# Kernel optimization log

Hardware: AMD Instinct MI355X
Metric: run time of the kernel (lower is better)

The kernel has to match this reference:

```python
import jax, jax.numpy as jnp
import numpy as np

N = 6144      # total residues (12 complexes x 512)
SEG = 512
NC = 14       # atom channels per residue
E = 64        # embed_size
HD = 128      # hidden_size
C = 25        # num_classes
K = 9         # k_neighbors
L = 3         # n_layers
ROUNDS = 3    # iter_round


def _forward(X, S, batch_id, embed, W_in, b_in, channel_w, eW1, eb1, eW2, eb2, cW1, cb1, cW2, cb2, nW1, nb1, nW2, nb2, mW1, mb1, mW2, mb2, oW1, ob1, oW2, ob2):
    n = X.shape[0]
    silu = jax.nn.silu
    # pairs in different complexes (or self) are never neighbors
    cross = (batch_id[:, None] != batch_id[None, :]) | jnp.eye(n, dtype=bool)
    Hmem = None
    H = None
    for t in range(ROUNDS):
        H0 = embed[S]                                    # residue embedding [N,E]
        if Hmem is not None:                             # keep_memory: memory_ffn(H_prev)
            m = silu(Hmem) @ mW1 + mb1
            H0 = H0 + (silu(m) @ mW2 + mb2)
        H = H0 @ W_in + b_in                             # [N,HD]
        # dynamic KNN edge construction on current CA coordinates (_knn_edges)
        ca = X[:, 1]                                     # [N,3]
        d2 = jnp.sum((ca[:, None, :] - ca[None, :, :]) ** 2, -1)
        d2 = jnp.where(cross, 1e9, d2)
        _, nbr = jax.lax.top_k(-d2, K)                   # [N,K] neighbor indices
        for l in range(L):                               # AMEGNN / AMEncoder layers
            Hj = H[nbr]                                  # gather [N,K,HD]
            Xj = X[nbr]                                  # gather [N,K,NC,3]
            diff = X[:, None] - Xj                       # [N,K,NC,3]
            # channel-weighted radial feature
            radial = jnp.einsum('nkcd,nkcd,c->nk', diff, diff, channel_w)[..., None]
            Hi = jnp.broadcast_to(H[:, None], Hj.shape)
            ein = jnp.concatenate([Hi, Hj, radial], -1)  # [N,K,2HD+1]
            msg = silu(silu(ein @ eW1[l] + eb1[l]) @ eW2[l] + eb2[l])
            scale = silu(msg @ cW1[l] + cb1[l]) @ cW2[l] + cb2[l]     # [N,K,1]
            X = X + jnp.mean(diff * scale[..., None], axis=1)        # equivariant coord update
            agg = jnp.sum(msg, axis=1)                   # scatter-sum over neighbors [N,HD]
            H = H + silu(jnp.concatenate([H, agg], -1) @ nW1[l] + nb1[l]) @ nW2[l] + nb2[l]
        Hmem = H
    logits = silu(silu(H) @ oW1 + ob1) @ oW2 + ob2       # ffn_residue
    return logits, X


def setup_inputs() -> dict:
    key = jax.random.key(0)
    ks = jax.random.split(key, 16)
    r = lambda i, shape, s=0.05: jax.random.normal(ks[i], shape, dtype=jnp.float32) * s
    return {
        'X': jax.random.normal(ks[0], (N, NC, 3), dtype=jnp.float32) * 3.0,
        'S': jax.random.randint(ks[1], (N,), 0, C),
        'batch_id': jnp.arange(N, dtype=jnp.int32) // SEG,
        'embed': r(2, (C, E), 1.0),
        'W_in': r(3, (E, HD)), 'b_in': jnp.zeros((HD,), jnp.float32),
        'channel_w': jax.random.uniform(ks[4], (NC,), dtype=jnp.float32),
        'eW1': r(5, (L, 2 * HD + 1, HD)), 'eb1': jnp.zeros((L, HD), jnp.float32),
        'eW2': r(6, (L, HD, HD)), 'eb2': jnp.zeros((L, HD), jnp.float32),
        'cW1': r(7, (L, HD, HD)), 'cb1': jnp.zeros((L, HD), jnp.float32),
        'cW2': r(8, (L, HD, 1)), 'cb2': jnp.zeros((L, 1), jnp.float32),
        'nW1': r(9, (L, 2 * HD, HD)), 'nb1': jnp.zeros((L, HD), jnp.float32),
        'nW2': r(10, (L, HD, HD)), 'nb2': jnp.zeros((L, HD), jnp.float32),
        'mW1': r(11, (HD, HD)), 'mb1': jnp.zeros((HD,), jnp.float32),
        'mW2': r(12, (HD, E)), 'mb2': jnp.zeros((E,), jnp.float32),
        'oW1': r(13, (HD, HD)), 'ob1': jnp.zeros((HD,), jnp.float32),
        'oW2': r(14, (HD, C)), 'ob2': jnp.zeros((C,), jnp.float32),
    }


def reference(X, S, batch_id, embed, W_in, b_in, channel_w, eW1, eb1, eW2, eb2, cW1, cb1, cW2, cb2, nW1, nb1, nW2, nb2, mW1, mb1, mW2, mb2, oW1, ob1, oW2, ob2):
    return _forward(X, S, batch_id, embed, W_in, b_in, channel_w, eW1, eb1, eW2, eb2, cW1, cb1, cW2, cb2, nW1, nb1, nW2, nb2, mW1, mb1, mW2, mb2, oW1, ob1, oW2, ob2)
```

## Files before the change

kernel.cpp:

```cpp
#include <hip/hip_runtime.h>
#include <hip/hip_bf16.h>
#include <math.h>

#define NNODE 6144
#define SEG   512
#define NCH   14
#define XD    42
#define ED    64
#define HD    128
#define NCLS  25
#define KN    9
#define NPB   7
#define ROWS  64
#define EDGE_BLOCKS ((NNODE + NPB - 1) / NPB)

typedef __attribute__((ext_vector_type(8))) short short8;
typedef __attribute__((ext_vector_type(4))) short short4v;
typedef __attribute__((ext_vector_type(4))) float f32x4;

__device__ __forceinline__ float silu_f(float x) {
  return x / (1.0f + __expf(-x));
}
__device__ __forceinline__ short f2bf(float x) {
  __hip_bfloat16 h = __float2bfloat16(x);
  return __builtin_bit_cast(short, h);
}
__device__ __forceinline__ unsigned pkbf(float lo, float hi) {
  return (unsigned)(unsigned short)f2bf(lo)
       | ((unsigned)(unsigned short)f2bf(hi) << 16);
}
__device__ __forceinline__ float bf2f(short s) {
  unsigned u = ((unsigned)(unsigned short)s) << 16;
  return __builtin_bit_cast(float, u);
}
__device__ __forceinline__ f32x4 mfma16(short8 a, short8 b, f32x4 c) {
  return __builtin_amdgcn_mfma_f32_16x16x32_bf16(a, b, c, 0, 0, 0);
}
__device__ __forceinline__ int swz128(int row, int col) {
  return row * 128 + (col ^ ((row & 7) << 3));
}
__device__ __forceinline__ int swz256(int row, int col) {
  return row * 256 + (col ^ ((row & 7) << 3));
}
__device__ __forceinline__ int swz64(int row, int col) {
  return row * 64 + (col ^ ((row & 7) << 3));
}

#define EXOFF 344064
#define WBF_SHORTS (EXOFF + 32768)

__global__ __launch_bounds__(256) void prep_weights(
    const float* __restrict__ eW1, const float* __restrict__ eW2,
    const float* __restrict__ cW1, const float* __restrict__ nW1,
    const float* __restrict__ nW2, const float* __restrict__ mW1,
    const float* __restrict__ mW2, const float* __restrict__ W_in,
    short* __restrict__ out)
{
  const int idx = blockIdx.x * 256 + threadIdx.x;
  if (blockIdx.y == 15) {
    if (idx < 16384) {
      const int n = idx >> 7, k = idx & 127;
      out[EXOFF + idx] = f2bf(mW1[k * HD + n]);
    } else if (idx < 24576) {
      const int local = idx - 16384;
      const int n = local >> 7, k = local & 127;
      out[EXOFF + 16384 + local] = f2bf(mW2[k * ED + n]);
    } else if (idx < 32768) {
      const int local = idx - 24576;
      const int n = local >> 6, k = local & 63;
      out[EXOFF + 24576 + local] = f2bf(W_in[k * HD + n]);
    }
    return;
  }
  const int mat = blockIdx.y % 5, l = blockIdx.y / 5;
  const int K = (mat == 0 || mat == 3) ? 256 : 128;
  if (idx >= K * 128) return;
  const int n = idx / K, k = idx - n * K;
  const float* src;
  switch (mat) {
    case 0: src = eW1 + (size_t)l * 257 * 128; break;
    case 1: src = eW2 + (size_t)l * 128 * 128; break;
    case 2: src = cW1 + (size_t)l * 128 * 128; break;
    case 3: src = nW1 + (size_t)l * 256 * 128; break;
    default: src = nW2 + (size_t)l * 128 * 128; break;
  }
  const int dofs[5] = {0, 32768, 49152, 65536, 98304};
  out[(size_t)l * 114688 + dofs[mat] + idx] = f2bf(src[k * 128 + n]);
}

__global__ void copy_kernel(const float* __restrict__ src, float* __restrict__ dst, int n) {
  int i = blockIdx.x * blockDim.x + threadIdx.x;
  if (i < n) dst[i] = src[i];
}

__global__ __launch_bounds__(512) void h_init_mfma(
    const float* __restrict__ embed, const int* __restrict__ S,
    const short* __restrict__ W_inT, const float* __restrict__ b_in,
    const float* __restrict__ Hmem,
    const short* __restrict__ mW1T, const float* __restrict__ mb1,
    const short* __restrict__ mW2T, const float* __restrict__ mb2,
    const short* __restrict__ W1T0,
    float* __restrict__ Hout, short* __restrict__ PQ0)
{
  __shared__ __align__(16) short A[16 * HD];
  __shared__ __align__(16) short Bu[16 * HD];
  __shared__ __align__(16) short h0B[16 * ED];
  __shared__ __align__(16) short HB[16 * HD];
  const int t = threadIdx.x;
  const int m0 = blockIdx.x * 16;
  const int wid = t >> 6, lane = t & 63, lr = lane & 15, lk = lane >> 4;

  if (Hmem) {
    {
      const int r = t >> 5, c4 = t & 31;
      const float4 v = ((const float4*)Hmem)[(size_t)(m0 + r) * 32 + c4];
      uint2 u;
      u.x = pkbf(silu_f(v.x), silu_f(v.y));
      u.y = pkbf(silu_f(v.z), silu_f(v.w));
      *(uint2*)&A[swz128(r, c4 * 4)] = u;
    }
    __syncthreads();
    {
      f32x4 acc[2] = {};
#pragma unroll
      for (int ks = 0; ks < 4; ++ks) {
        const int k0 = ks * 32 + lk * 8;
        const short8 a = *(const short8*)&A[swz128(lr, k0)];
#pragma unroll
        for (int ni = 0; ni < 2; ++ni) {
          const int c = (wid * 2 + ni) * 16 + lr;
          acc[ni] = mfma16(a, *(const short8*)(mW1T + c * 128 + k0), acc[ni]);
        }
      }
#pragma unroll
      for (int ni = 0; ni < 2; ++ni) {
        const int col = (wid * 2 + ni) * 16 + lr;
        const float bias = mb1[col];
#pragma unroll
        for (int g = 0; g < 4; ++g)
          Bu[swz128(lk * 4 + g, col)] = f2bf(silu_f(acc[ni][g] + bias));
      }
    }
    __syncthreads();
    if (wid < 4) {
      f32x4 acc = {};
#pragma unroll
      for (int ks = 0; ks < 4; ++ks) {
        const int k0 = ks * 32 + lk * 8;
        const short8 a = *(const short8*)&Bu[swz128(lr, k0)];
        const int c = wid * 16 + lr;
        acc = mfma16(a, *(const short8*)(mW2T + c * 128 + k0), acc);
      }
      const int col = wid * 16 + lr;
      const float bias = mb2[col];
#pragma unroll
      for (int g = 0; g < 4; ++g) {
        const int row = lk * 4 + g;
        h0B[swz64(row, col)] = f2bf(embed[S[m0 + row] * ED + col] + acc[g] + bias);
      }
    }
  } else {
    for (int idx = t; idx < 16 * ED; idx += 512) {
      const int row = idx >> 6, col = idx & 63;
      h0B[swz64(row, col)] = f2bf(embed[S[m0 + row] * ED + col]);
    }
  }
  __syncthreads();
  {
    f32x4 acc = {};
#pragma unroll
    for (int ks = 0; ks < 2; ++ks) {
      const int k0 = ks * 32 + lk * 8;
      const short8 a = *(const short8*)&h0B[swz64(lr, k0)];
      const int c = wid * 16 + lr;
      acc = mfma16(a, *(const short8*)(W_inT + c * 64 + k0), acc);
    }
    const int col = wid * 16 + lr;
    const float bias = b_in[col];
#pragma unroll
    for (int g = 0; g < 4; ++g) {
      const int row = lk * 4 + g;
      const float hv = acc[g] + bias;
      Hout[(size_t)(m0 + row) * HD + col] = hv;
      HB[swz128(row, col)] = f2bf(hv);
    }
  }
  __syncthreads();
  {
    f32x4 acc[2] = {};
#pragma unroll
    for (int ks = 0; ks < 4; ++ks) {
      const int k0 = ks * 32 + lk * 8;
      const short8 a = *(const short8*)&HB[swz128(lr, k0)];
#pragma unroll
      for (int ni = 0; ni < 2; ++ni) {
        const int c = (wid * 2 + ni) * 16 + lr;
        const short* bp = (c < HD) ? (W1T0 + c * 256 + k0)
                                   : (W1T0 + (c - HD) * 256 + HD + k0);
        acc[ni] = mfma16(a, *(const short8*)bp, acc[ni]);
      }
    }
#pragma unroll
    for (int ni = 0; ni < 2; ++ni) {
      const int c = (wid * 2 + ni) * 16 + lr;
#pragma unroll
      for (int g = 0; g < 4; ++g)
        PQ0[(size_t)(m0 + lk * 4 + g) * 256 + c] = f2bf(acc[ni][g]);
    }
  }
}

__global__ __launch_bounds__(512) void knn_kernel(const float* __restrict__ X,
                                                  int* __restrict__ nbr)
{
  const int w = threadIdx.x >> 6, lane = threadIdx.x & 63;
  const int i = blockIdx.x * 8 + w;
  const int base = (i / SEG) * SEG;

  const float cx = X[i * XD + 3], cy = X[i * XD + 4], cz = X[i * XD + 5];
  float dv[8];
  int   di[8];
#pragma unroll
  for (int q = 0; q < 8; ++q) {
    const int j = base + lane + q * 64;
    float dx = __fsub_rn(cx, X[j * XD + 3]);
    float dy = __fsub_rn(cy, X[j * XD + 4]);
    float dz = __fsub_rn(cz, X[j * XD + 5]);
    float d2 = __fadd_rn(__fadd_rn(__fmul_rn(dx, dx), __fmul_rn(dy, dy)), __fmul_rn(dz, dz));
    if (j == i) d2 = 1e9f;
    dv[q] = d2; di[q] = j;
  }
  for (int it = 0; it < KN; ++it) {
    float bv = dv[0]; int bi = di[0];
#pragma unroll
    for (int q = 1; q < 8; ++q)
      if (dv[q] < bv || (dv[q] == bv && di[q] < bi)) { bv = dv[q]; bi = di[q]; }
#pragma unroll
    for (int m = 1; m < 64; m <<= 1) {
      float ov = __shfl_xor(bv, m, 64);
      int   oi = __shfl_xor(bi, m, 64);
      if (ov < bv || (ov == bv && oi < bi)) { bv = ov; bi = oi; }
    }
    if (lane == 0) nbr[i * KN + it] = bi;
    const int rel = bi - base;
    const int oq = rel >> 6;
#pragma unroll
    for (int q = 0; q < 8; ++q)
      if (q == oq && (rel & 63) == lane) dv[q] = 3e38f;
  }
}

__global__ __launch_bounds__(512) void edge_layer_kernel(
    const float* __restrict__ Hin,  float* __restrict__ Hout,
    const float* __restrict__ Xin,  float* __restrict__ Xout,
    const int*   __restrict__ nbr,  const float* __restrict__ channel_w,
    const short* __restrict__ PQ,
    const float* __restrict__ eW1,  const float* __restrict__ eb1,
    const float* __restrict__ eb2,  const float* __restrict__ cb1,
    const float* __restrict__ cW2,  const float* __restrict__ cb2,
    const float* __restrict__ nb1,  const float* __restrict__ nb2,
    const short* __restrict__ W2T,  const short* __restrict__ C1T,
    const short* __restrict__ N1T,  const short* __restrict__ N2T,
    const short* __restrict__ W1Tn, short* __restrict__ PQn)
{
  __shared__ __align__(16) short bufA[ROWS * HD];
  __shared__ __align__(16) short bufB[ROWS * HD];
  __shared__ __align__(16) short nodeA[NPB * 256];
  __shared__ __align__(16) short uT[NPB * HD];
  __shared__ float scalePart[ROWS][4];
  __shared__ int   nbrS[ROWS];
  short* houtB = bufA;

  const int t  = threadIdx.x;
  const int n0 = blockIdx.x * NPB;
  const int nvalid = (NNODE - n0 < NPB) ? (NNODE - n0) : NPB;
  const int evalid = nvalid * KN;

  {
    const int row  = t >> 3;
    const int part = t & 7;
    const bool rvalid = row < evalid;
    const int nd = row / KN;
    const int jn = rvalid ? nbr[n0 * KN + row] : n0;
    if (part == 0) nbrS[row] = jn;

    float r = 0.f;
    {
      const float* xi = Xin + (size_t)(n0 + ((nd < nvalid) ? nd : 0)) * XD;
      const float* xj = Xin + (size_t)jn * XD;
#pragma unroll
      for (int ii = 0; ii < 6; ++ii) {
        const int e = part + ii * 8;
        if (e < XD) {
          float d = 0.f;
          if (rvalid) d = xi[e] - xj[e];
          r = fmaf(channel_w[e / 3] * d, d, r);
        }
      }
    }
    r += __shfl_xor(r, 1, 64);
    r += __shfl_xor(r, 2, 64);
    r += __shfl_xor(r, 4, 64);

    if (t < NPB * (HD / 4)) {
      const int r2 = t >> 5, c4 = t & 31;
      float4 v = make_float4(0.f, 0.f, 0.f, 0.f);
      if (r2 < nvalid) v = ((const float4*)Hin)[(size_t)(n0 + r2) * 32 + c4];
      uint2 u;
      u.x = pkbf(v.x, v.y);
      u.y = pkbf(v.z, v.w);
      *(uint2*)&nodeA[swz256(r2, c4 * 4)] = u;
    }

    const int inode = n0 + ((nd < nvalid) ? nd : 0);
    const short4v* PQv = (const short4v*)PQ;
    const float4* w2564 = (const float4*)(eW1 + 256 * HD);
    const float4* eb14 = (const float4*)eb1;
#pragma unroll
    for (int ii = 0; ii < 4; ++ii) {
      const int c4 = part + ii * 8;
      const short4v ps = PQv[(size_t)inode * 64 + c4];
      const short4v qs = PQv[(size_t)jn * 64 + 32 + c4];
      const float4 w = w2564[c4];
      const float4 bb = eb14[c4];
      uint2 u;
      u.x = pkbf(silu_f(bf2f(ps.x) + bf2f(qs.x) + r * w.x + bb.x),
                 silu_f(bf2f(ps.y) + bf2f(qs.y) + r * w.y + bb.y));
      u.y = pkbf(silu_f(bf2f(ps.z) + bf2f(qs.z) + r * w.z + bb.z),
                 silu_f(bf2f(ps.w) + bf2f(qs.w) + r * w.w + bb.w));
      *(uint2*)&bufA[swz128(row, c4 * 4)] = u;
    }
  }
  __syncthreads();

  const int wid  = t >> 6;
  const int lane = t & 63;
  const int m2 = wid >> 2;
  const int n2 = wid & 3;
  const int lr = lane & 15;
  const int lk = lane >> 4;
  const int rA0 = (m2 * 2) * 16 + lr;
  const int rA1 = rA0 + 16;

  {
    f32x4 acc[2][2] = {};
    const short* b0p = W2T + ((n2 * 2) * 16 + lr) * 128;
    const short* b1p = b0p + 16 * 128;
#pragma unroll
    for (int ks = 0; ks < 4; ++ks) {
      const int k0 = ks * 32 + lk * 8;
      const short8 a0 = *(const short8*)&bufA[swz128(rA0, k0)];
      const short8 a1 = *(const short8*)&bufA[swz128(rA1, k0)];
      const short8 b0 = *(const short8*)(b0p + k0);
      const short8 b1 = *(const short8*)(b1p + k0);
      acc[0][0] = mfma16(a0, b0, acc[0][0]);
      acc[0][1] = mfma16(a0, b1, acc[0][1]);
      acc[1][0] = mfma16(a1, b0, acc[1][0]);
      acc[1][1] = mfma16(a1, b1, acc[1][1]);
    }
#pragma unroll
    for (int ni = 0; ni < 2; ++ni) {
      const int col = (n2 * 2 + ni) * 16 + lr;
      const float bias = eb2[col];
#pragma unroll
      for (int mi = 0; mi < 2; ++mi) {
        const int rb = (m2 * 2 + mi) * 16 + lk * 4;
#pragma unroll
        for (int g = 0; g < 4; ++g)
          bufB[swz128(rb + g, col)] = f2bf(silu_f(acc[mi][ni][g] + bias));
      }
    }
  }
  __syncthreads();

  {
    f32x4 acc[2][2] = {};
    const short* b0p = C1T + ((n2 * 2) * 16 + lr) * 128;
    const short* b1p = b0p + 16 * 128;
#pragma unroll
    for (int ks = 0; ks < 4; ++ks) {
      const int k0 = ks * 32 + lk * 8;
      const short8 a0 = *(const short8*)&bufB[swz128(rA0, k0)];
      const short8 a1 = *(const short8*)&bufB[swz128(rA1, k0)];
      const short8 b0 = *(const short8*)(b0p + k0);
      const short8 b1 = *(const short8*)(b1p + k0);
      acc[0][0] = mfma16(a0, b0, acc[0][0]);
      acc[0][1] = mfma16(a0, b1, acc[0][1]);
      acc[1][0] = mfma16(a1, b0, acc[1][0]);
      acc[1][1] = mfma16(a1, b1, acc[1][1]);
    }
    float p[2][4];
#pragma unroll
    for (int mi = 0; mi < 2; ++mi)
#pragma unroll
      for (int g = 0; g < 4; ++g) p[mi][g] = 0.f;
#pragma unroll
    for (int ni = 0; ni < 2; ++ni) {
      const int col = (n2 * 2 + ni) * 16 + lr;
      const float bias = cb1[col];
      const float wv = cW2[col];
#pragma unroll
      for (int mi = 0; mi < 2; ++mi)
#pragma unroll
        for (int g = 0; g < 4; ++g)
          p[mi][g] = fmaf(silu_f(acc[mi][ni][g] + bias), wv, p[mi][g]);
    }
#pragma unroll
    for (int m = 1; m < 16; m <<= 1) {
#pragma unroll
      for (int mi = 0; mi < 2; ++mi)
#pragma unroll
        for (int g = 0; g < 4; ++g)
          p[mi][g] += __shfl_xor(p[mi][g], m, 64);
    }
    if (lr == 0) {
#pragma unroll
      for (int mi = 0; mi < 2; ++mi)
#pragma unroll
        for (int g = 0; g < 4; ++g)
          scalePart[(m2 * 2 + mi) * 16 + lk * 4 + g][n2] = p[mi][g];
    }
  }
  if (t < NPB * (HD / 2)) {
    const int r2 = t >> 6, cp = (t & 63) * 2;
    float v0 = 0.f, v1 = 0.f;
#pragma unroll
    for (int k = 0; k < KN; ++k) {
      const unsigned w = *(const unsigned*)&bufB[swz128(r2 * KN + k, cp)];
      v0 += bf2f((short)(w & 0xffffu));
      v1 += bf2f((short)(w >> 16));
    }
    if (r2 >= nvalid) { v0 = 0.f; v1 = 0.f; }
    *(unsigned*)&nodeA[swz256(r2, cp + HD)] = pkbf(v0, v1);
  }
  __syncthreads();

  {
    f32x4 acc = {};
    const short* bp = N1T + (wid * 16 + lr) * 256;
#pragma unroll
    for (int ks = 0; ks < 8; ++ks) {
      const int k0 = ks * 32 + lk * 8;
      short8 a = {0, 0, 0, 0, 0, 0, 0, 0};
      if (lr < NPB) a = *(const short8*)&nodeA[swz256(lr, k0)];
      const short8 b = *(const short8*)(bp + k0);
      acc = mfma16(a, b, acc);
    }
    const int col = wid * 16 + lr;
    const float bias = nb1[col];
#pragma unroll
    for (int g = 0; g < 4; ++g) {
      const int orow = lk * 4 + g;
      if (orow < NPB) uT[swz128(orow, col)] = f2bf(silu_f(acc[g] + bias));
    }
  }
  if (t < NPB * XD) {
    const int nd = t / XD, e = t - nd * XD;
    if (nd < nvalid) {
      const float c2 = cb2[0];
      const float xi = Xin[(size_t)n0 * XD + t];
      float a = 0.f;
#pragma unroll
      for (int k = 0; k < KN; ++k) {
        const int r = nd * KN + k;
        const float sc = ((scalePart[r][0] + scalePart[r][1])
                        + (scalePart[r][2] + scalePart[r][3])) + c2;
        a = fmaf(xi - Xin[(size_t)nbrS[r] * XD + e], sc, a);
      }
      Xout[(size_t)n0 * XD + t] = xi + a / 9.0f;
    }
  }
  __syncthreads();

  {
    f32x4 acc = {};
    const short* bp = N2T + (wid * 16 + lr) * 128;
#pragma unroll
    for (int ks = 0; ks < 4; ++ks) {
      const int k0 = ks * 32 + lk * 8;
      short8 a = {0, 0, 0, 0, 0, 0, 0, 0};
      if (lr < NPB) a = *(const short8*)&uT[swz128(lr, k0)];
      const short8 b = *(const short8*)(bp + k0);
      acc = mfma16(a, b, acc);
    }
    const int col = wid * 16 + lr;
    const float bias = nb2[col];
#pragma unroll
    for (int g = 0; g < 4; ++g) {
      const int row = lk * 4 + g;
      if (row < nvalid) {
        const float hv = Hin[(size_t)(n0 + row) * HD + col] + acc[g] + bias;
        Hout[(size_t)(n0 + row) * HD + col] = hv;
        if (W1Tn) houtB[swz128(row, col)] = f2bf(hv);
      }
    }
  }

  if (W1Tn) {
    __syncthreads();
    f32x4 acc[2] = {};
#pragma unroll
    for (int ks = 0; ks < 4; ++ks) {
      const int k0 = ks * 32 + lk * 8;
      short8 a = {0, 0, 0, 0, 0, 0, 0, 0};
      if (lr < NPB) a = *(const short8*)&houtB[swz128(lr, k0)];
#pragma unroll
      for (int ni = 0; ni < 2; ++ni) {
        const int c = (wid * 2 + ni) * 16 + lr;
        const short* bp = (c < HD) ? (W1Tn + c * 256 + k0)
                                   : (W1Tn + (c - HD) * 256 + HD + k0);
        acc[ni] = mfma16(a, *(const short8*)bp, acc[ni]);
      }
    }
#pragma unroll
    for (int ni = 0; ni < 2; ++ni) {
      const int c = (wid * 2 + ni) * 16 + lr;
#pragma unroll
      for (int g = 0; g < 4; ++g) {
        const int row = lk * 4 + g;
        if (row < nvalid) PQn[(size_t)(n0 + row) * 256 + c] = f2bf(acc[ni][g]);
      }
    }
  }
}

__global__ __launch_bounds__(128) void out_kernel(
    const float* __restrict__ H, const float* __restrict__ X,
    const float* __restrict__ oW1, const float* __restrict__ ob1,
    const float* __restrict__ oW2, const float* __restrict__ ob2,
    float* __restrict__ out)
{
  __shared__ float hs[HD];
  __shared__ float u[HD];
  const int i = blockIdx.x, j = threadIdx.x;

  hs[j] = silu_f(H[i * HD + j]);
  __syncthreads();
  float a0 = 0.f, a1 = 0.f, a2 = 0.f, a3 = 0.f;
  for (int k = 0; k < HD; k += 4) {
    a0 = fmaf(hs[k + 0], oW1[(k + 0) * HD + j], a0);
    a1 = fmaf(hs[k + 1], oW1[(k + 1) * HD + j], a1);
    a2 = fmaf(hs[k + 2], oW1[(k + 2) * HD + j], a2);
    a3 = fmaf(hs[k + 3], oW1[(k + 3) * HD + j], a3);
  }
  u[j] = silu_f(ob1[j] + ((a0 + a1) + (a2 + a3)));
  __syncthreads();
  if (j < NCLS) {
    float o0 = 0.f, o1 = 0.f, o2 = 0.f, o3 = 0.f;
    for (int k = 0; k < HD; k += 4) {
      o0 = fmaf(u[k + 0], oW2[(k + 0) * NCLS + j], o0);
      o1 = fmaf(u[k + 1], oW2[(k + 1) * NCLS + j], o1);
      o2 = fmaf(u[k + 2], oW2[(k + 2) * NCLS + j], o2);
      o3 = fmaf(u[k + 3], oW2[(k + 3) * NCLS + j], o3);
    }
    out[i * NCLS + j] = ob2[j] + ((o0 + o1) + (o2 + o3));
  }
  if (j < XD) out[NNODE * NCLS + i * XD + j] = X[i * XD + j];
}

extern "C" void kernel_launch(void* const* d_in, const int* in_sizes, int n_in,
                              void* d_out, int out_size, void* d_ws, size_t ws_size,
                              hipStream_t stream)
{
  const float* X0       = (const float*)d_in[0];
  const int*   S        = (const int*)  d_in[1];
  const float* embed    = (const float*)d_in[3];
  const float* W_in     = (const float*)d_in[4];
  const float* b_in     = (const float*)d_in[5];
  const float* channelw = (const float*)d_in[6];
  const float* eW1      = (const float*)d_in[7];
  const float* eb1      = (const float*)d_in[8];
  const float* eW2      = (const float*)d_in[9];
  const float* eb2      = (const float*)d_in[10];
  const float* cW1      = (const float*)d_in[11];
  const float* cb1      = (const float*)d_in[12];
  const float* cW2      = (const float*)d_in[13];
  const float* cb2      = (const float*)d_in[14];
  const float* nW1      = (const float*)d_in[15];
  const float* nb1      = (const float*)d_in[16];
  const float* nW2      = (const float*)d_in[17];
  const float* nb2      = (const float*)d_in[18];
  const float* mW1      = (const float*)d_in[19];
  const float* mb1      = (const float*)d_in[20];
  const float* mW2      = (const float*)d_in[21];
  const float* mb2      = (const float*)d_in[22];
  const float* oW1      = (const float*)d_in[23];
  const float* ob1      = (const float*)d_in[24];
  const float* oW2      = (const float*)d_in[25];
  const float* ob2      = (const float*)d_in[26];

  char* ws = (char*)d_ws;
  const size_t HBYTES = (size_t)NNODE * HD * sizeof(float);
  const size_t XBYTES = (size_t)NNODE * XD * sizeof(float);
  const size_t NBRB   = (size_t)NNODE * KN * sizeof(int);
  const size_t WBFB   = (size_t)WBF_SHORTS * sizeof(short);
  const size_t PQB    = (size_t)NNODE * 256 * sizeof(short);
  float* Hb[2] = { (float*)(ws), (float*)(ws + HBYTES) };
  float* Xb[2] = { (float*)(ws + 2 * HBYTES), (float*)(ws + 2 * HBYTES + XBYTES) };
  int*   nbr   = (int*)(ws + 2 * HBYTES + 2 * XBYTES);
  short* Wbf   = (short*)(ws + 2 * HBYTES + 2 * XBYTES + NBRB);
  short* PQb[2] = { (short*)(ws + 2 * HBYTES + 2 * XBYTES + NBRB + WBFB),
                    (short*)(ws + 2 * HBYTES + 2 * XBYTES + NBRB + WBFB + PQB) };

  prep_weights<<<dim3(128, 16), 256, 0, stream>>>(eW1, eW2, cW1, nW1, nW2,
                                                  mW1, mW2, W_in, Wbf);
  copy_kernel<<<(NNODE * XD + 255) / 256, 256, 0, stream>>>(X0, Xb[0], NNODE * XD);

  int hc = 0, xc = 0;
  for (int t = 0; t < 3; ++t) {
    const float* Hmem = (t == 0) ? nullptr : Hb[hc];
    h_init_mfma<<<NNODE / 16, 512, 0, stream>>>(
        embed, S, Wbf + EXOFF + 24576, b_in, Hmem,
        Wbf + EXOFF, mb1, Wbf + EXOFF + 16384, mb2,
        Wbf , Hb[hc ^ 1], PQb[0]);
    hc ^= 1;
    knn_kernel<<<NNODE / 8, 512, 0, stream>>>(Xb[xc], nbr);
    for (int l = 0; l < 3; ++l) {
      const short* Wl = Wbf + (size_t)l * 114688;
      const short* Wn = (l < 2) ? (Wbf + (size_t)(l + 1) * 114688) : nullptr;
      const short* pqr = (l == 1) ? PQb[1] : PQb[0];
      short* pqw = (l == 0) ? PQb[1] : ((l == 1) ? PQb[0] : nullptr);
      edge_layer_kernel<<<EDGE_BLOCKS, 512, 0, stream>>>(
          Hb[hc], Hb[hc ^ 1], Xb[xc], Xb[xc ^ 1], nbr, channelw, pqr,
          eW1 + (size_t)l * 257 * HD, eb1 + (size_t)l * HD,
          eb2 + (size_t)l * HD,  cb1 + (size_t)l * HD,
          cW2 + (size_t)l * HD,  cb2 + (size_t)l,
          nb1 + (size_t)l * HD,  nb2 + (size_t)l * HD,
          Wl + 32768, Wl + 49152, Wl + 65536, Wl + 98304,
          Wn, pqw);
      hc ^= 1; xc ^= 1;
    }
  }
  out_kernel<<<NNODE, HD, 0, stream>>>(Hb[hc], Xb[xc], oW1, ob1, oW2, ob2, (float*)d_out);
}
```

Measured before the change: 535.5 us.

## Shrink edge-layer blocks to 3 nodes, 256 threads, and rebalance MFMA tiling

Edge-layer blocks now handle 3 nodes (27 edge rows padded to 32) with 4 waves instead of 7 nodes (63 rows padded to 64) with 8 waves. The MFMA work split is remapped so each wave owns wider column strips, and the boundary checks go away because 6144 divides by 3 evenly. This cuts padding waste, raises block count and occupancy, and lowers LDS use per block. In exchange the per-block weight loads are amortised over fewer nodes, and the node-level MFMAs, which use only 3 of 16 A rows, waste more tensor work. SiLU also now uses a reciprocal multiply in place of a divide.

Result: slower. 702.6 us (+31.2%).

```diff
diff --git a/kernel.cpp b/kernel.cpp
--- a/kernel.cpp
+++ b/kernel.cpp
@@ -10,16 +10,16 @@
 #define HD    128
 #define NCLS  25
 #define KN    9
-#define NPB   7
-#define ROWS  64
-#define EDGE_BLOCKS ((NNODE + NPB - 1) / NPB)
+#define NPB   3
+#define ROWS  32
+#define EDGE_BLOCKS (NNODE / NPB)
 
 typedef __attribute__((ext_vector_type(8))) short short8;
 typedef __attribute__((ext_vector_type(4))) short short4v;
 typedef __attribute__((ext_vector_type(4))) float f32x4;
 
 __device__ __forceinline__ float silu_f(float x) {
-  return x / (1.0f + __expf(-x));
+  return x * __frcp_rn(1.0f + __expf(-x));
 }
 __device__ __forceinline__ short f2bf(float x) {
   __hip_bfloat16 h = __float2bfloat16(x);
@@ -250,7 +250,7 @@
   }
 }
 
-__global__ __launch_bounds__(512) void edge_layer_kernel(
+__global__ __launch_bounds__(256) void edge_layer_kernel(
     const float* __restrict__ Hin,  float* __restrict__ Hout,
     const float* __restrict__ Xin,  float* __restrict__ Xout,
     const int*   __restrict__ nbr,  const float* __restrict__ channel_w,
@@ -273,8 +273,15 @@
 
   const int t  = threadIdx.x;
   const int n0 = blockIdx.x * NPB;
-  const int nvalid = (NNODE - n0 < NPB) ? (NNODE - n0) : NPB;
-  const int evalid = nvalid * KN;
+  const int nvalid = NPB;
+  const int evalid = NPB * KN;
+
+  const int wid  = t >> 6;
+  const int lane = t & 63;
+  const int lr = lane & 15;
+  const int lk = lane >> 4;
+  const int rA0 = lr;
+  const int rA1 = 16 + lr;
 
   {
     const int row  = t >> 3;
@@ -304,8 +311,7 @@
 
     if (t < NPB * (HD / 4)) {
       const int r2 = t >> 5, c4 = t & 31;
-      float4 v = make_float4(0.f, 0.f, 0.f, 0.f);
-      if (r2 < nvalid) v = ((const float4*)Hin)[(size_t)(n0 + r2) * 32 + c4];
+      const float4 v = ((const float4*)Hin)[(size_t)(n0 + r2) * 32 + c4];
       uint2 u;
       u.x = pkbf(v.x, v.y);
       u.y = pkbf(v.z, v.w);
@@ -333,18 +339,9 @@
   }
   __syncthreads();
 
-  const int wid  = t >> 6;
-  const int lane = t & 63;
-  const int m2 = wid >> 2;
-  const int n2 = wid & 3;
-  const int lr = lane & 15;
-  const int lk = lane >> 4;
-  const int rA0 = (m2 * 2) * 16 + lr;
-  const int rA1 = rA0 + 16;
-
   {
     f32x4 acc[2][2] = {};
-    const short* b0p = W2T + ((n2 * 2) * 16 + lr) * 128;
+    const short* b0p = W2T + ((wid * 2) * 16 + lr) * 128;
     const short* b1p = b0p + 16 * 128;
 #pragma unroll
     for (int ks = 0; ks < 4; ++ks) {
@@ -360,11 +357,11 @@
     }
 #pragma unroll
     for (int ni = 0; ni < 2; ++ni) {
-      const int col = (n2 * 2 + ni) * 16 + lr;
+      const int col = (wid * 2 + ni) * 16 + lr;
       const float bias = eb2[col];
 #pragma unroll
       for (int mi = 0; mi < 2; ++mi) {
-        const int rb = (m2 * 2 + mi) * 16 + lk * 4;
+        const int rb = mi * 16 + lk * 4;
 #pragma unroll
         for (int g = 0; g < 4; ++g)
           bufB[swz128(rb + g, col)] = f2bf(silu_f(acc[mi][ni][g] + bias));
@@ -375,7 +372,7 @@
 
   {
     f32x4 acc[2][2] = {};
-    const short* b0p = C1T + ((n2 * 2) * 16 + lr) * 128;
+    const short* b0p = C1T + ((wid * 2) * 16 + lr) * 128;
     const short* b1p = b0p + 16 * 128;
 #pragma unroll
     for (int ks = 0; ks < 4; ++ks) {
@@ -396,7 +393,7 @@
       for (int g = 0; g < 4; ++g) p[mi][g] = 0.f;
 #pragma unroll
     for (int ni = 0; ni < 2; ++ni) {
-      const int col = (n2 * 2 + ni) * 16 + lr;
+      const int col = (wid * 2 + ni) * 16 + lr;
       const float bias = cb1[col];
       const float wv = cW2[col];
 #pragma unroll
@@ -418,7 +415,7 @@
       for (int mi = 0; mi < 2; ++mi)
 #pragma unroll
         for (int g = 0; g < 4; ++g)
-          scalePart[(m2 * 2 + mi) * 16 + lk * 4 + g][n2] = p[mi][g];
+          scalePart[mi * 16 + lk * 4 + g][wid] = p[mi][g];
     }
   }
   if (t < NPB * (HD / 2)) {
@@ -430,91 +427,96 @@
       v0 += bf2f((short)(w & 0xffffu));
       v1 += bf2f((short)(w >> 16));
     }
-    if (r2 >= nvalid) { v0 = 0.f; v1 = 0.f; }
     *(unsigned*)&nodeA[swz256(r2, cp + HD)] = pkbf(v0, v1);
   }
   __syncthreads();
 
   {
-    f32x4 acc = {};
-    const short* bp = N1T + (wid * 16 + lr) * 256;
+    f32x4 acc[2] = {};
+    const short* bp0 = N1T + ((wid * 2) * 16 + lr) * 256;
+    const short* bp1 = bp0 + 16 * 256;
 #pragma unroll
     for (int ks = 0; ks < 8; ++ks) {
       const int k0 = ks * 32 + lk * 8;
       short8 a = {0, 0, 0, 0, 0, 0, 0, 0};
       if (lr < NPB) a = *(const short8*)&nodeA[swz256(lr, k0)];
-      const short8 b = *(const short8*)(bp + k0);
-      acc = mfma16(a, b, acc);
-    }
-    const int col = wid * 16 + lr;
-    const float bias = nb1[col];
-#pragma unroll
-    for (int g = 0; g < 4; ++g) {
-      const int orow = lk * 4 + g;
-      if (orow < NPB) uT[swz128(orow, col)] = f2bf(silu_f(acc[g] + bias));
+      acc[0] = mfma16(a, *(const short8*)(bp0 + k0), acc[0]);
+      acc[1] = mfma16(a, *(const short8*)(bp1 + k0), acc[1]);
+    }
+#pragma unroll
+    for (int ni = 0; ni < 2; ++ni) {
+      const int col = (wid * 2 + ni) * 16 + lr;
+      const float bias = nb1[col];
+#pragma unroll
+      for (int g = 0; g < 4; ++g) {
+        const int orow = lk * 4 + g;
+        if (orow < NPB) uT[swz128(orow, col)] = f2bf(silu_f(acc[ni][g] + bias));
+      }
     }
   }
   if (t < NPB * XD) {
     const int nd = t / XD, e = t - nd * XD;
-    if (nd < nvalid) {
-      const float c2 = cb2[0];
-      const float xi = Xin[(size_t)n0 * XD + t];
-      float a = 0.f;
-#pragma unroll
-      for (int k = 0; k < KN; ++k) {
-        const int r = nd * KN + k;
-        const float sc = ((scalePart[r][0] + scalePart[r][1])
-                        + (scalePart[r][2] + scalePart[r][3])) + c2;
-        a = fmaf(xi - Xin[(size_t)nbrS[r] * XD + e], sc, a);
-      }
-      Xout[(size_t)n0 * XD + t] = xi + a / 9.0f;
-    }
+    const float c2 = cb2[0];
+    const float xi = Xin[(size_t)n0 * XD + t];
+    float a = 0.f;
+#pragma unroll
+    for (int k = 0; k < KN; ++k) {
+      const int r = nd * KN + k;
+      const float sc = ((scalePart[r][0] + scalePart[r][1])
+                      + (scalePart[r][2] + scalePart[r][3])) + c2;
+      a = fmaf(xi - Xin[(size_t)nbrS[r] * XD + e], sc, a);
+    }
+    Xout[(size_t)n0 * XD + t] = xi + a / 9.0f;
   }
   __syncthreads();
 
   {
-    f32x4 acc = {};
-    const short* bp = N2T + (wid * 16 + lr) * 128;
+    f32x4 acc[2] = {};
+    const short* bp0 = N2T + ((wid * 2) * 16 + lr) * 128;
+    const short* bp1 = bp0 + 16 * 128;
 #pragma unroll
     for (int ks = 0; ks < 4; ++ks) {
       const int k0 = ks * 32 + lk * 8;
       short8 a = {0, 0, 0, 0, 0, 0, 0, 0};
       if (lr < NPB) a = *(const short8*)&uT[swz128(lr, k0)];
-      const short8 b = *(const short8*)(bp + k0);
-      acc = mfma16(a, b, acc);
-    }
-    const int col = wid * 16 + lr;
-    const float bias = nb2[col];
-#pragma unroll
-    for (int g = 0; g < 4; ++g) {
-      const int row = lk * 4 + g;
-      if (row < nvalid) {
-        const float hv = Hin[(size_t)(n0 + row) * HD + col] + acc[g] + bias;
-        Hout[(size_t)(n0 + row) * HD + col] = hv;
-        if (W1Tn) houtB[swz128(row, col)] = f2bf(hv);
+      acc[0] = mfma16(a, *(const short8*)(bp0 + k0), acc[0]);
+      acc[1] = mfma16(a, *(const short8*)(bp1 + k0), acc[1]);
+    }
+#pragma unroll
+    for (int ni = 0; ni < 2; ++ni) {
+      const int col = (wid * 2 + ni) * 16 + lr;
+      const float bias = nb2[col];
+#pragma unroll
+      for (int g = 0; g < 4; ++g) {
+        const int row = lk * 4 + g;
+        if (row < nvalid) {
+          const float hv = Hin[(size_t)(n0 + row) * HD + col] + acc[ni][g] + bias;
+          Hout[(size_t)(n0 + row) * HD + col] = hv;
+          if (W1Tn) houtB[swz128(row, col)] = f2bf(hv);
+        }
       }
     }
   }
 
   if (W1Tn) {
     __syncthreads();
-    f32x4 acc[2] = {};
+    f32x4 acc[4] = {};
 #pragma unroll
     for (int ks = 0; ks < 4; ++ks) {
       const int k0 = ks * 32 + lk * 8;
       short8 a = {0, 0, 0, 0, 0, 0, 0, 0};
       if (lr < NPB) a = *(const short8*)&houtB[swz128(lr, k0)];
 #pragma unroll
-      for (int ni = 0; ni < 2; ++ni) {
-        const int c = (wid * 2 + ni) * 16 + lr;
+      for (int ni = 0; ni < 4; ++ni) {
+        const int c = (wid * 4 + ni) * 16 + lr;
         const short* bp = (c < HD) ? (W1Tn + c * 256 + k0)
                                    : (W1Tn + (c - HD) * 256 + HD + k0);
         acc[ni] = mfma16(a, *(const short8*)bp, acc[ni]);
       }
     }
 #pragma unroll
-    for (int ni = 0; ni < 2; ++ni) {
-      const int c = (wid * 2 + ni) * 16 + lr;
+    for (int ni = 0; ni < 4; ++ni) {
+      const int c = (wid * 4 + ni) * 16 + lr;
 #pragma unroll
       for (int g = 0; g < 4; ++g) {
         const int row = lk * 4 + g;
@@ -620,7 +622,7 @@
       const short* Wn = (l < 2) ? (Wbf + (size_t)(l + 1) * 114688) : nullptr;
       const short* pqr = (l == 1) ? PQb[1] : PQb[0];
       short* pqw = (l == 0) ? PQb[1] : ((l == 1) ? PQb[0] : nullptr);
-      edge_layer_kernel<<<EDGE_BLOCKS, 512, 0, stream>>>(
+      edge_layer_kernel<<<EDGE_BLOCKS, 256, 0, stream>>>(
           Hb[hc], Hb[hc ^ 1], Xb[xc], Xb[xc ^ 1], nbr, channelw, pqr,
           eW1 + (size_t)l * 257 * HD, eb1 + (size_t)l * HD,
           eb2 + (size_t)l * HD,  cb1 + (size_t)l * HD,
```

## Fold neighbor aggregation into node MLP via linearity and use 6 nodes per block

Applied to the files above, without the earlier changes.

The edge layer kernel now computes the node MLP's first layer by splitting it into an H part (computed up front from global memory) and an aggregated-message part. The second part is obtained by running the N1 weight MFMA on every edge row alongside the C1 GEMM and then summing per node with shuffles. This uses linearity of the matmul in place of an explicit bf16 sum over the 9 neighbors in shared memory, removing a sync and the nodeA buffer. Nodes per block drop to 6 with a padded 32-row layout so each half of the 64-row tile holds 3 nodes and there are no partial blocks. The trade-off is more MFMA work per edge row, fewer node rows per block, and a reciprocal-based silu.

Result: slower. 626.4 us (+17.0%).

```diff
diff --git a/kernel.cpp b/kernel.cpp
--- a/kernel.cpp
+++ b/kernel.cpp
@@ -10,16 +10,16 @@
 #define HD    128
 #define NCLS  25
 #define KN    9
-#define NPB   7
+#define NPB   6
 #define ROWS  64
-#define EDGE_BLOCKS ((NNODE + NPB - 1) / NPB)
+#define EDGE_BLOCKS (NNODE / NPB)
 
 typedef __attribute__((ext_vector_type(8))) short short8;
 typedef __attribute__((ext_vector_type(4))) short short4v;
 typedef __attribute__((ext_vector_type(4))) float f32x4;
 
 __device__ __forceinline__ float silu_f(float x) {
-  return x / (1.0f + __expf(-x));
+  return x * __frcp_rn(1.0f + __expf(-x));
 }
 __device__ __forceinline__ short f2bf(float x) {
   __hip_bfloat16 h = __float2bfloat16(x);
@@ -38,9 +38,6 @@
 }
 __device__ __forceinline__ int swz128(int row, int col) {
   return row * 128 + (col ^ ((row & 7) << 3));
-}
-__device__ __forceinline__ int swz256(int row, int col) {
-  return row * 256 + (col ^ ((row & 7) << 3));
 }
 __device__ __forceinline__ int swz64(int row, int col) {
   return row * 64 + (col ^ ((row & 7) << 3));
@@ -265,7 +262,7 @@
 {
   __shared__ __align__(16) short bufA[ROWS * HD];
   __shared__ __align__(16) short bufB[ROWS * HD];
-  __shared__ __align__(16) short nodeA[NPB * 256];
+  __shared__ float uPre[NPB * HD];
   __shared__ __align__(16) short uT[NPB * HD];
   __shared__ float scalePart[ROWS][4];
   __shared__ int   nbrS[ROWS];
@@ -273,20 +270,49 @@
 
   const int t  = threadIdx.x;
   const int n0 = blockIdx.x * NPB;
-  const int nvalid = (NNODE - n0 < NPB) ? (NNODE - n0) : NPB;
-  const int evalid = nvalid * KN;
+
+  const int wid  = t >> 6;
+  const int lane = t & 63;
+  const int m2 = wid >> 2;
+  const int n2 = wid & 3;
+  const int lr = lane & 15;
+  const int lk = lane >> 4;
+  const int rA0 = m2 * 32 + lr;
+  const int rA1 = rA0 + 16;
 
   {
+    f32x4 accHi = {};
+    const short* bHi = N1T + (wid * 16 + lr) * 256;
+#pragma unroll
+    for (int ks = 0; ks < 4; ++ks) {
+      const int k0 = ks * 32 + lk * 8;
+      short8 a = {0, 0, 0, 0, 0, 0, 0, 0};
+      if (lr < NPB) {
+        const float* hp = Hin + (size_t)(n0 + lr) * HD + k0;
+        const float4 v0 = *(const float4*)hp;
+        const float4 v1 = *(const float4*)(hp + 4);
+        a[0] = f2bf(v0.x); a[1] = f2bf(v0.y); a[2] = f2bf(v0.z); a[3] = f2bf(v0.w);
+        a[4] = f2bf(v1.x); a[5] = f2bf(v1.y); a[6] = f2bf(v1.z); a[7] = f2bf(v1.w);
+      }
+      accHi = mfma16(a, *(const short8*)(bHi + k0), accHi);
+    }
+#pragma unroll
+    for (int g = 0; g < 4; ++g) {
+      const int row = lk * 4 + g;
+      if (row < NPB) uPre[row * HD + wid * 16 + lr] = accHi[g];
+    }
+
     const int row  = t >> 3;
     const int part = t & 7;
-    const bool rvalid = row < evalid;
-    const int nd = row / KN;
-    const int jn = rvalid ? nbr[n0 * KN + row] : n0;
+    int nd = 0; bool rvalid = false; int kk = 0;
+    if (row < 27)               { nd = row / 9;            kk = row % 9;        rvalid = true; }
+    else if (row >= 32 && row < 59) { nd = 3 + (row - 32) / 9; kk = (row - 32) % 9; rvalid = true; }
+    const int jn = rvalid ? nbr[(size_t)(n0 + nd) * KN + kk] : n0;
     if (part == 0) nbrS[row] = jn;
 
     float r = 0.f;
     {
-      const float* xi = Xin + (size_t)(n0 + ((nd < nvalid) ? nd : 0)) * XD;
+      const float* xi = Xin + (size_t)(n0 + nd) * XD;
       const float* xj = Xin + (size_t)jn * XD;
 #pragma unroll
       for (int ii = 0; ii < 6; ++ii) {
@@ -302,17 +328,7 @@
     r += __shfl_xor(r, 2, 64);
     r += __shfl_xor(r, 4, 64);
 
-    if (t < NPB * (HD / 4)) {
-      const int r2 = t >> 5, c4 = t & 31;
-      float4 v = make_float4(0.f, 0.f, 0.f, 0.f);
-      if (r2 < nvalid) v = ((const float4*)Hin)[(size_t)(n0 + r2) * 32 + c4];
-      uint2 u;
-      u.x = pkbf(v.x, v.y);
-      u.y = pkbf(v.z, v.w);
-      *(uint2*)&nodeA[swz256(r2, c4 * 4)] = u;
-    }
-
-    const int inode = n0 + ((nd < nvalid) ? nd : 0);
+    const int inode = n0 + nd;
     const short4v* PQv = (const short4v*)PQ;
     const float4* w2564 = (const float4*)(eW1 + 256 * HD);
     const float4* eb14 = (const float4*)eb1;
@@ -333,15 +349,6 @@
   }
   __syncthreads();
 
-  const int wid  = t >> 6;
-  const int lane = t & 63;
-  const int m2 = wid >> 2;
-  const int n2 = wid & 3;
-  const int lr = lane & 15;
-  const int lk = lane >> 4;
-  const int rA0 = (m2 * 2) * 16 + lr;
-  const int rA1 = rA0 + 16;
-
   {
     f32x4 acc[2][2] = {};
     const short* b0p = W2T + ((n2 * 2) * 16 + lr) * 128;
@@ -374,100 +381,98 @@
   __syncthreads();
 
   {
-    f32x4 acc[2][2] = {};
+    f32x4 accS[2][2] = {};
+    f32x4 accU[2][2] = {};
     const short* b0p = C1T + ((n2 * 2) * 16 + lr) * 128;
     const short* b1p = b0p + 16 * 128;
+    const short* u0p = N1T + ((n2 * 2) * 16 + lr) * 256 + 128;
+    const short* u1p = u0p + 16 * 256;
 #pragma unroll
     for (int ks = 0; ks < 4; ++ks) {
       const int k0 = ks * 32 + lk * 8;
       const short8 a0 = *(const short8*)&bufB[swz128(rA0, k0)];
       const short8 a1 = *(const short8*)&bufB[swz128(rA1, k0)];
-      const short8 b0 = *(const short8*)(b0p + k0);
-      const short8 b1 = *(const short8*)(b1p + k0);
-      acc[0][0] = mfma16(a0, b0, acc[0][0]);
-      acc[0][1] = mfma16(a0, b1, acc[0][1]);
-      acc[1][0] = mfma16(a1, b0, acc[1][0]);
-      acc[1][1] = mfma16(a1, b1, acc[1][1]);
-    }
-    float p[2][4];
-#pragma unroll
-    for (int mi = 0; mi < 2; ++mi)
-#pragma unroll
-      for (int g = 0; g < 4; ++g) p[mi][g] = 0.f;
-#pragma unroll
-    for (int ni = 0; ni < 2; ++ni) {
-      const int col = (n2 * 2 + ni) * 16 + lr;
-      const float bias = cb1[col];
-      const float wv = cW2[col];
+      accS[0][0] = mfma16(a0, *(const short8*)(b0p + k0), accS[0][0]);
+      accS[0][1] = mfma16(a0, *(const short8*)(b1p + k0), accS[0][1]);
+      accS[1][0] = mfma16(a1, *(const short8*)(b0p + k0), accS[1][0]);
+      accS[1][1] = mfma16(a1, *(const short8*)(b1p + k0), accS[1][1]);
+      accU[0][0] = mfma16(a0, *(const short8*)(u0p + k0), accU[0][0]);
+      accU[0][1] = mfma16(a0, *(const short8*)(u1p + k0), accU[0][1]);
+      accU[1][0] = mfma16(a1, *(const short8*)(u0p + k0), accU[1][0]);
+      accU[1][1] = mfma16(a1, *(const short8*)(u1p + k0), accU[1][1]);
+    }
+    {
+      float p[2][4];
 #pragma unroll
       for (int mi = 0; mi < 2; ++mi)
 #pragma unroll
-        for (int g = 0; g < 4; ++g)
-          p[mi][g] = fmaf(silu_f(acc[mi][ni][g] + bias), wv, p[mi][g]);
-    }
-#pragma unroll
-    for (int m = 1; m < 16; m <<= 1) {
+        for (int g = 0; g < 4; ++g) p[mi][g] = 0.f;
+#pragma unroll
+      for (int ni = 0; ni < 2; ++ni) {
+        const int col = (n2 * 2 + ni) * 16 + lr;
+        const float bias = cb1[col];
+        const float wv = cW2[col];
+#pragma unroll
+        for (int mi = 0; mi < 2; ++mi)
+#pragma unroll
+          for (int g = 0; g < 4; ++g)
+            p[mi][g] = fmaf(silu_f(accS[mi][ni][g] + bias), wv, p[mi][g]);
+      }
+#pragma unroll
+      for (int m = 1; m < 16; m <<= 1) {
+#pragma unroll
+        for (int mi = 0; mi < 2; ++mi)
+#pragma unroll
+          for (int g = 0; g < 4; ++g)
+            p[mi][g] += __shfl_xor(p[mi][g], m, 64);
+      }
+      if (lr == 0) {
+#pragma unroll
+        for (int mi = 0; mi < 2; ++mi)
+#pragma unroll
+          for (int g = 0; g < 4; ++g)
+            scalePart[m2 * 32 + mi * 16 + lk * 4 + g][n2] = p[mi][g];
+      }
+    }
+    {
+      float part[2][3];
+#pragma unroll
+      for (int ni = 0; ni < 2; ++ni)
+#pragma unroll
+        for (int j = 0; j < 3; ++j) part[ni][j] = 0.f;
 #pragma unroll
       for (int mi = 0; mi < 2; ++mi)
 #pragma unroll
-        for (int g = 0; g < 4; ++g)
-          p[mi][g] += __shfl_xor(p[mi][g], m, 64);
-    }
-    if (lr == 0) {
-#pragma unroll
-      for (int mi = 0; mi < 2; ++mi)
-#pragma unroll
-        for (int g = 0; g < 4; ++g)
-          scalePart[(m2 * 2 + mi) * 16 + lk * 4 + g][n2] = p[mi][g];
-    }
-  }
-  if (t < NPB * (HD / 2)) {
-    const int r2 = t >> 6, cp = (t & 63) * 2;
-    float v0 = 0.f, v1 = 0.f;
-#pragma unroll
-    for (int k = 0; k < KN; ++k) {
-      const unsigned w = *(const unsigned*)&bufB[swz128(r2 * KN + k, cp)];
-      v0 += bf2f((short)(w & 0xffffu));
-      v1 += bf2f((short)(w >> 16));
-    }
-    if (r2 >= nvalid) { v0 = 0.f; v1 = 0.f; }
-    *(unsigned*)&nodeA[swz256(r2, cp + HD)] = pkbf(v0, v1);
-  }
-  __syncthreads();
-
-  {
-    f32x4 acc = {};
-    const short* bp = N1T + (wid * 16 + lr) * 256;
-#pragma unroll
-    for (int ks = 0; ks < 8; ++ks) {
-      const int k0 = ks * 32 + lk * 8;
-      short8 a = {0, 0, 0, 0, 0, 0, 0, 0};
-      if (lr < NPB) a = *(const short8*)&nodeA[swz256(lr, k0)];
-      const short8 b = *(const short8*)(bp + k0);
-      acc = mfma16(a, b, acc);
-    }
-    const int col = wid * 16 + lr;
-    const float bias = nb1[col];
-#pragma unroll
-    for (int g = 0; g < 4; ++g) {
-      const int orow = lk * 4 + g;
-      if (orow < NPB) uT[swz128(orow, col)] = f2bf(silu_f(acc[g] + bias));
-    }
-  }
-  if (t < NPB * XD) {
-    const int nd = t / XD, e = t - nd * XD;
-    if (nd < nvalid) {
-      const float c2 = cb2[0];
-      const float xi = Xin[(size_t)n0 * XD + t];
-      float a = 0.f;
-#pragma unroll
-      for (int k = 0; k < KN; ++k) {
-        const int r = nd * KN + k;
-        const float sc = ((scalePart[r][0] + scalePart[r][1])
-                        + (scalePart[r][2] + scalePart[r][3])) + c2;
-        a = fmaf(xi - Xin[(size_t)nbrS[r] * XD + e], sc, a);
-      }
-      Xout[(size_t)n0 * XD + t] = xi + a / 9.0f;
+        for (int g = 0; g < 4; ++g) {
+          const int lrow = mi * 16 + lk * 4 + g;
+#pragma unroll
+          for (int j = 0; j < 3; ++j) {
+            const bool in = (lrow >= j * 9) && (lrow < j * 9 + 9);
+#pragma unroll
+            for (int ni = 0; ni < 2; ++ni)
+              part[ni][j] += in ? accU[mi][ni][g] : 0.f;
+          }
+        }
+#pragma unroll
+      for (int m = 16; m < 64; m <<= 1)
+#pragma unroll
+        for (int ni = 0; ni < 2; ++ni)
+#pragma unroll
+          for (int j = 0; j < 3; ++j)
+            part[ni][j] += __shfl_xor(part[ni][j], m, 64);
+      if (lk == 0) {
+#pragma unroll
+        for (int ni = 0; ni < 2; ++ni) {
+          const int col = (n2 * 2 + ni) * 16 + lr;
+          const float bias = nb1[col];
+#pragma unroll
+          for (int j = 0; j < 3; ++j) {
+            const int node = m2 * 3 + j;
+            const float uv = silu_f(uPre[node * HD + col] + part[ni][j] + bias);
+            uT[swz128(node, col)] = f2bf(uv);
+          }
+        }
+      }
     }
   }
   __syncthreads();
@@ -480,20 +485,33 @@
       const int k0 = ks * 32 + lk * 8;
       short8 a = {0, 0, 0, 0, 0, 0, 0, 0};
       if (lr < NPB) a = *(const short8*)&uT[swz128(lr, k0)];
-      const short8 b = *(const short8*)(bp + k0);
-      acc = mfma16(a, b, acc);
+      acc = mfma16(a, *(const short8*)(bp + k0), acc);
     }
     const int col = wid * 16 + lr;
     const float bias = nb2[col];
 #pragma unroll
     for (int g = 0; g < 4; ++g) {
       const int row = lk * 4 + g;
-      if (row < nvalid) {
+      if (row < NPB) {
         const float hv = Hin[(size_t)(n0 + row) * HD + col] + acc[g] + bias;
         Hout[(size_t)(n0 + row) * HD + col] = hv;
         if (W1Tn) houtB[swz128(row, col)] = f2bf(hv);
       }
     }
+  }
+  if (t < NPB * XD) {
+    const int nd = t / XD, e = t - nd * XD;
+    const float c2 = cb2[0];
+    const float xi = Xin[(size_t)n0 * XD + t];
+    float a = 0.f;
+#pragma unroll
+    for (int k = 0; k < KN; ++k) {
+      const int r = (nd < 3) ? (nd * 9 + k) : (32 + (nd - 3) * 9 + k);
+      const float sc = ((scalePart[r][0] + scalePart[r][1])
+                      + (scalePart[r][2] + scalePart[r][3])) + c2;
+      a = fmaf(xi - Xin[(size_t)nbrS[r] * XD + e], sc, a);
+    }
+    Xout[(size_t)n0 * XD + t] = xi + a / 9.0f;
   }
 
   if (W1Tn) {
@@ -518,7 +536,7 @@
 #pragma unroll
       for (int g = 0; g < 4; ++g) {
         const int row = lk * 4 + g;
-        if (row < nvalid) PQn[(size_t)(n0 + row) * 256 + c] = f2bf(acc[ni][g]);
+        if (row < NPB) PQn[(size_t)(n0 + row) * 256 + c] = f2bf(acc[ni][g]);
       }
     }
   }
```
